# Optimization experiments

Hardware: AMD Instinct MI355X
Metric: run time of the kernel (lower is better)

The kernel has to match this reference:

```python
import jax, jax.numpy as jnp
import numpy as np
import math

B, S, D, H = 2, 2048, 1024, 16
DK = D // H


def setup_inputs() -> dict:
    key = jax.random.key(0)
    ks = jax.random.split(key, 12)
    std = 1.0 / math.sqrt(D)
    inp = {
        "q": jax.random.normal(ks[0], (B, S, D), jnp.float32),
        "k": jax.random.normal(ks[1], (B, S, D), jnp.float32),
        "v": jax.random.normal(ks[2], (B, S, D), jnp.float32),
        # causal mask, broadcast over batch and heads
        "mask": jnp.tril(jnp.ones((S, S), jnp.int32))[None, None, :, :],
        "wq": jax.random.normal(ks[3], (D, D), jnp.float32) * std,
        "bq": jax.random.normal(ks[4], (D,), jnp.float32) * std,
        "wk": jax.random.normal(ks[5], (D, D), jnp.float32) * std,
        "bk": jax.random.normal(ks[6], (D,), jnp.float32) * std,
        "wv": jax.random.normal(ks[7], (D, D), jnp.float32) * std,
        "bv": jax.random.normal(ks[8], (D,), jnp.float32) * std,
        "wo": jax.random.normal(ks[9], (D, D), jnp.float32) * std,
        "bo": jax.random.normal(ks[10], (D,), jnp.float32) * std,
    }
    return inp


def _split_heads(x):
    # [B,S,D] -> [B,H,S,DK]
    b, s, _ = x.shape
    return x.reshape(b, s, H, DK).transpose(0, 2, 1, 3)


def reference(q, k, v, mask, wq, bq, wk, bk, wv, bv, wo, bo):
    # nn.Linear: y = x @ W^T + b
    query = _split_heads(q @ wq.T + bq)
    key_h = _split_heads(k @ wk.T + bk)
    value = _split_heads(v @ wv.T + bv)

    scale = 1.0 / math.sqrt(DK)
    scores = jnp.einsum("bhqd,bhkd->bhqk", query, key_h) * scale  # [B,H,S,S]
    scores = jnp.where(mask == 0, jnp.float32(-1e9), scores)
    attn = jax.nn.softmax(scores, axis=-1)  # dropout p=0.0 -> identity

    x = jnp.einsum("bhqk,bhkd->bhqd", attn, value)  # [B,H,S,DK]
    x = x.transpose(0, 2, 1, 3).reshape(q.shape[0], -1, H * DK)  # [B,S,D]
    return x @ wo.T + bo
```

## Files before the change

kernel.cpp:

```cpp
#include <hip/hip_runtime.h>

#define B_SZ    2
#define S_LEN   2048
#define D_MODEL 1024
#define H_NUM   16
#define DK_H    64
#define M_ROWS  (B_SZ * S_LEN)

typedef __attribute__((ext_vector_type(8))) short  short8;
typedef __attribute__((ext_vector_type(4))) short  short4v;
typedef __attribute__((ext_vector_type(4))) float  floatx4;

__device__ __forceinline__ short f2b(float f) {
    union { float f; unsigned u; } x; x.f = f;
    unsigned u = x.u + 0x7fffu + ((x.u >> 16) & 1u);
    return (short)(u >> 16);
}

typedef __attribute__((address_space(1))) const unsigned int gu32;
typedef __attribute__((address_space(3))) unsigned int       lu32;
__device__ __forceinline__ void gload_lds16(const short* g, short* l) {
    __builtin_amdgcn_global_load_lds((gu32*)g, (lu32*)l, 16, 0, 0);
}

#define QSCALE 0.18033688011112042f
#define SM_SHIFT 12.0f

__global__ void cvt_all_kernel(const float* __restrict__ xq, const float* __restrict__ xk,
                               const float* __restrict__ xv, const float* __restrict__ wq,
                               const float* __restrict__ wk, const float* __restrict__ wv,
                               const float* __restrict__ wo,
                               short* __restrict__ oxq, short* __restrict__ oxk,
                               short* __restrict__ oxv, short* __restrict__ owq,
                               short* __restrict__ owk, short* __restrict__ owv,
                               short* __restrict__ owo)
{
    const int y = blockIdx.y;
    const float* in;
    short* out;
    switch (y) {
        case 0: in = xq; out = oxq; break;
        case 1: in = xk; out = oxk; break;
        case 2: in = xv; out = oxv; break;
        case 3: in = wq; out = owq; break;
        case 4: in = wk; out = owk; break;
        case 5: in = wv; out = owv; break;
        default: in = wo; out = owo; break;
    }
    if (y < 3) {
        int base = blockIdx.x * 1024 + threadIdx.x * 4;
        for (int p = 0; p < 4; ++p) {
            int i = base + p * 1048576;
            float4 v = *(const float4*)(in + i);
            short4v r;
            r[0] = f2b(v.x); r[1] = f2b(v.y); r[2] = f2b(v.z); r[3] = f2b(v.w);
            *(short4v*)(out + i) = r;
        }
    } else {
        int f = blockIdx.x * 256 + (int)threadIdx.x;
        if (blockIdx.x < 512) {
            int n4 = f >> 11, rem = f & 2047;
            int k8 = rem >> 4, nl = rem & 15;
            const float* src = in + (size_t)(n4 * 16 + nl) * D_MODEL + k8 * 8;
            float4 v0 = *(const float4*)(src);
            float4 v1 = *(const float4*)(src + 4);
            short8 r;
            r[0] = f2b(v0.x); r[1] = f2b(v0.y); r[2] = f2b(v0.z); r[3] = f2b(v0.w);
            r[4] = f2b(v1.x); r[5] = f2b(v1.y); r[6] = f2b(v1.z); r[7] = f2b(v1.w);
            *(short8*)(out + (size_t)f * 8) = r;
        }
    }
}

__global__ __launch_bounds__(256, 2)
void gemm_qkv_kernel(const short* __restrict__ xq, const short* __restrict__ xk,
                     const short* __restrict__ xv,
                     const short* __restrict__ wq, const short* __restrict__ wk,
                     const short* __restrict__ wv,
                     const float* __restrict__ bq, const float* __restrict__ bk,
                     const float* __restrict__ bv,
                     short* __restrict__ Qp, short* __restrict__ Kp, short* __restrict__ Vt)
{
    __shared__ short sa[2][128 * 64];

    const int which = blockIdx.y >> 3;
    const short* A    = (which == 0) ? xq : (which == 1) ? xk : xv;
    const short* W    = (which == 0) ? wq : (which == 1) ? wk : wv;
    const float* bias = (which == 0) ? bq : (which == 1) ? bk : bv;
    const float scale = (which == 0) ? QSCALE : 1.0f;

    const int nb = (blockIdx.y & 7) * 128;
    const int m0 = blockIdx.x * 128;
    const int t = threadIdx.x, wave = t >> 6, lane = t & 63;
    const int quad = lane >> 4, l16 = lane & 15;
    const int wm = (wave & 1) * 64, wn = (wave >> 1) * 64;

    const int rs = t >> 3;
    const int cl = (t & 7) ^ (rs & 7);
    const short* Asrc = A + (size_t)(m0 + rs) * D_MODEL + cl * 8;
    short* sd0 = &sa[0][t * 8];
    short* sd1 = &sa[1][t * 8];

#define STAGE_A(dst, k0) do { _Pragma("unroll")                                \
    for (int j_ = 0; j_ < 4; ++j_)                                             \
        gload_lds16(Asrc + (size_t)j_ * 32 * D_MODEL + (k0),                   \
                    (dst) + j_ * 2048); } while (0)

    int a_off[4][2];
#pragma unroll
    for (int i = 0; i < 4; ++i) {
        int ar = wm + i * 16 + l16;
#pragma unroll
        for (int ks = 0; ks < 2; ++ks)
            a_off[i][ks] = ar * 64 + (((ks * 4 + quad) ^ (ar & 7)) * 8);
    }

    const short* Wt = W + ((size_t)((nb + wn) >> 4) * 128 + quad) * 128 + l16 * 8;

#define LOADB(dst, k0) do { _Pragma("unroll")                                  \
    for (int nt_ = 0; nt_ < 4; ++nt_)                                          \
        dst[nt_] = *(const short8*)(Wt + nt_ * 16384 + (k0) * 16); } while (0)

    short8 bfA[4], bfB[4];
    STAGE_A(sd0, 0);
    LOADB(bfA, 0);
    __syncthreads();

    floatx4 acc[4][4] = {};
#pragma unroll 1
    for (int k0 = 0; k0 < D_MODEL; k0 += 64) {
        const int p = (k0 >> 6) & 1;
        const short* cur = &sa[p][0];
        if (k0 + 64 < D_MODEL) STAGE_A(p ? sd0 : sd1, k0 + 64);
        LOADB(bfB, k0 + 32);

        short8 af[4][2];
#pragma unroll
        for (int mt = 0; mt < 4; ++mt) {
            af[mt][0] = *(const short8*)(cur + a_off[mt][0]);
            af[mt][1] = *(const short8*)(cur + a_off[mt][1]);
        }
#pragma unroll
        for (int mt = 0; mt < 4; ++mt)
#pragma unroll
            for (int nt = 0; nt < 4; ++nt)
                acc[mt][nt] = __builtin_amdgcn_mfma_f32_16x16x32_bf16(af[mt][0], bfA[nt], acc[mt][nt], 0, 0, 0);
        if (k0 + 64 < D_MODEL) LOADB(bfA, k0 + 64);
#pragma unroll
        for (int mt = 0; mt < 4; ++mt)
#pragma unroll
            for (int nt = 0; nt < 4; ++nt)
                acc[mt][nt] = __builtin_amdgcn_mfma_f32_16x16x32_bf16(af[mt][1], bfB[nt], acc[mt][nt], 0, 0, 0);
        __syncthreads();
    }
#undef STAGE_A
#undef LOADB

#pragma unroll
    for (int nt = 0; nt < 4; ++nt) {
        int ncol = nb + wn + nt * 16 + l16;
        int h = ncol >> 6, dk = ncol & 63;
        float bv_ = bias[ncol];
#pragma unroll
        for (int mt = 0; mt < 4; ++mt) {
            int mrow0 = m0 + wm + mt * 16 + quad * 4;
            int bb = mrow0 >> 11, s0 = mrow0 & (S_LEN - 1);
            if (which < 2) {
                short* Out = (which == 0) ? Qp : Kp;
#pragma unroll
                for (int r = 0; r < 4; ++r) {
                    float v = (acc[mt][nt][r] + bv_) * scale;
                    Out[(((size_t)bb * H_NUM + h) * S_LEN + (s0 + r)) * DK_H + dk] = f2b(v);
                }
            } else {
                int Sb = s0 & ~63, sb0_ = s0 & 63;
                size_t rowbase = (((size_t)bb * H_NUM + h) * DK_H + dk) * S_LEN + Sb;
#pragma unroll
                for (int r = 0; r < 4; ++r) {
                    int cc = sb0_ + r;
                    Vt[rowbase + ((cc & 15) * 4 + (cc >> 4))] = f2b(acc[mt][nt][r] + bv_);
                }
            }
        }
    }
}

__global__ __launch_bounds__(512, 4)
void attn_kernel(const short* __restrict__ Qp, const short* __restrict__ Kp,
                 const short* __restrict__ Vt, short* __restrict__ Xa)
{
    __shared__ short kbuf[2][64 * 64];
    __shared__ short vbuf[2][64 * 64];
    __shared__ short pl[8][16 * 72];

    const int lin = (int)(blockIdx.x + 16 * blockIdx.y);
    const int bh = lin & 31;
    const int j8 = (lin >> 5) & 7;
    const int tile = (lin >> 8) ? (15 - j8) : j8;

    const int t = threadIdx.x, wave = t >> 6, lane = t & 63;
    const int quad = lane >> 4, l16 = lane & 15;

    const short* Qb  = Qp + (size_t)bh * S_LEN * DK_H;
    const short* Kb  = Kp + (size_t)bh * S_LEN * DK_H;
    const short* Vtb = Vt + (size_t)bh * DK_H * S_LEN;

    const int q0 = tile * 128 + wave * 16;
    const int my_ktimax = 2 * tile + (wave >> 2);
    const int ktb = 2 * tile + 1;

    const int r0 = t >> 3, cs = t & 7;
    const int c0 = cs ^ (r0 & 7);
    const short* Kg = Kb + r0 * DK_H + c0 * 8;
    const short* Vg = Vtb + (size_t)r0 * S_LEN + c0 * 8;
    short* kl0 = &kbuf[0][t * 8]; short* kl1 = &kbuf[1][t * 8];
    short* vl0 = &vbuf[0][t * 8]; short* vl1 = &vbuf[1][t * 8];

    short8 qf[2];
#pragma unroll
    for (int ks = 0; ks < 2; ++ks)
        qf[ks] = *(const short8*)(Qb + (size_t)(q0 + l16) * DK_H + ks * 32 + quad * 8);

    short8 bl = {};
    if (l16 == 0) {
#pragma unroll
        for (int j = 0; j < 8; ++j) bl[j] = (short)0x3F80;
    }

    int fo[4][2];
#pragma unroll
    for (int nt = 0; nt < 4; ++nt)
#pragma unroll
        for (int ks = 0; ks < 2; ++ks) {
            int row = nt * 16 + l16;
            fo[nt][ks] = row * 64 + (((ks * 4 + quad) ^ (l16 & 7)) * 8);
        }

    floatx4 o[4] = {};
    floatx4 ol = {};
    short* plw = &pl[wave][0];
    const int qg = q0 + quad * 4;

    gload_lds16(Kg, kl0);
    gload_lds16(Vg, vl0);
    __syncthreads();

    for (int kti = 0; kti <= ktb; ++kti) {
        const short* kb = (kti & 1) ? &kbuf[1][0] : &kbuf[0][0];
        const short* vb = (kti & 1) ? &vbuf[1][0] : &vbuf[0][0];
        const int kbase = kti * 64;

        if (kti < ktb) {
            gload_lds16(Kg + (size_t)(kbase + 64) * DK_H, (kti & 1) ? kl0 : kl1);
            gload_lds16(Vg + (kbase + 64),                (kti & 1) ? vl0 : vl1);
        }

        if (kti <= my_ktimax) {
            short8 bkf[4][2];
#pragma unroll
            for (int nt = 0; nt < 4; ++nt)
#pragma unroll
                for (int ks = 0; ks < 2; ++ks)
                    bkf[nt][ks] = *(const short8*)(kb + fo[nt][ks]);

            floatx4 sc[4] = {};
#pragma unroll
            for (int nt = 0; nt < 4; ++nt)
#pragma unroll
                for (int ks = 0; ks < 2; ++ks)
                    sc[nt] = __builtin_amdgcn_mfma_f32_16x16x32_bf16(qf[ks], bkf[nt][ks], sc[nt], 0, 0, 0);

            if (kti == my_ktimax) {
#pragma unroll
                for (int nt = 0; nt < 4; ++nt) {
                    int key = kbase + nt * 16 + l16;
#pragma unroll
                    for (int r = 0; r < 4; ++r)
                        if (key > qg + r) sc[nt][r] = -1e30f;
                }
            }

#pragma unroll
            for (int r = 0; r < 4; ++r) {
                union { float f; unsigned u; } a0, a1, a2, a3;
                a0.f = exp2f(sc[0][r] - SM_SHIFT);
                a1.f = exp2f(sc[1][r] - SM_SHIFT);
                a2.f = exp2f(sc[2][r] - SM_SHIFT);
                a3.f = exp2f(sc[3][r] - SM_SHIFT);
                uint2 d;
                d.x = (a1.u & 0xffff0000u) | (a0.u >> 16);
                d.y = (a3.u & 0xffff0000u) | (a2.u >> 16);
                *(uint2*)(plw + (quad * 4 + r) * 72 + l16 * 4) = d;
            }

            short8 ap0 = *(const short8*)(plw + l16 * 72 + quad * 8);
            short8 ap1 = *(const short8*)(plw + l16 * 72 + 32 + quad * 8);

            short8 bvf[4][2];
#pragma unroll
            for (int nt = 0; nt < 4; ++nt)
#pragma unroll
                for (int ks = 0; ks < 2; ++ks)
                    bvf[nt][ks] = *(const short8*)(vb + fo[nt][ks]);

#pragma unroll
            for (int nt = 0; nt < 4; ++nt) {
                o[nt] = __builtin_amdgcn_mfma_f32_16x16x32_bf16(ap0, bvf[nt][0], o[nt], 0, 0, 0);
                o[nt] = __builtin_amdgcn_mfma_f32_16x16x32_bf16(ap1, bvf[nt][1], o[nt], 0, 0, 0);
            }
            ol = __builtin_amdgcn_mfma_f32_16x16x32_bf16(ap0, bl, ol, 0, 0, 0);
            ol = __builtin_amdgcn_mfma_f32_16x16x32_bf16(ap1, bl, ol, 0, 0, 0);
        }

        __syncthreads();
    }

    const int b_ = bh >> 4, h = bh & 15;
#pragma unroll
    for (int r = 0; r < 4; ++r) {
        float lsum = __shfl(ol[r], (lane & 48));
        float rinv = 1.0f / lsum;
        int srow = qg + r;
#pragma unroll
        for (int nt = 0; nt < 4; ++nt) {
            int col = h * 64 + nt * 16 + l16;
            Xa[((size_t)b_ * S_LEN + srow) * D_MODEL + col] = f2b(o[nt][r] * rinv);
        }
    }
}

__global__ __launch_bounds__(256, 2)
void gemm_out_kernel(const short* __restrict__ A, const short* __restrict__ W,
                     const float* __restrict__ bias, float* __restrict__ out)
{
    __shared__ short sa[2][128 * 64];

    const int nb = blockIdx.y * 64;
    const int m0 = blockIdx.x * 128;
    const int t = threadIdx.x, wave = t >> 6, lane = t & 63;
    const int quad = lane >> 4, l16 = lane & 15;
    const int wm = (wave & 1) * 64, wn = (wave >> 1) * 32;

    const int rs = t >> 3;
    const int cl = (t & 7) ^ (rs & 7);
    const short* Asrc = A + (size_t)(m0 + rs) * D_MODEL + cl * 8;
    short* sd0 = &sa[0][t * 8];
    short* sd1 = &sa[1][t * 8];

#define STAGE_A(dst, k0) do { _Pragma("unroll")                                \
    for (int j_ = 0; j_ < 4; ++j_)                                             \
        gload_lds16(Asrc + (size_t)j_ * 32 * D_MODEL + (k0),                   \
                    (dst) + j_ * 2048); } while (0)

    int a_off[4][2];
#pragma unroll
    for (int i = 0; i < 4; ++i) {
        int ar = wm + i * 16 + l16;
#pragma unroll
        for (int ks = 0; ks < 2; ++ks)
            a_off[i][ks] = ar * 64 + (((ks * 4 + quad) ^ (ar & 7)) * 8);
    }

    const short* Wt = W + ((size_t)((nb + wn) >> 4) * 128 + quad) * 128 + l16 * 8;

#define LOADB2(dst, k0) do { _Pragma("unroll")                                 \
    for (int nt_ = 0; nt_ < 2; ++nt_)                                          \
        dst[nt_] = *(const short8*)(Wt + nt_ * 16384 + (k0) * 16); } while (0)

    short8 bfA[2], bfB[2];
    STAGE_A(sd0, 0);
    LOADB2(bfA, 0);
    __syncthreads();

    floatx4 acc[4][2] = {};
#pragma unroll 1
    for (int k0 = 0; k0 < D_MODEL; k0 += 64) {
        const int p = (k0 >> 6) & 1;
        const short* cur = &sa[p][0];
        if (k0 + 64 < D_MODEL) STAGE_A(p ? sd0 : sd1, k0 + 64);
        LOADB2(bfB, k0 + 32);

        short8 af[4][2];
#pragma unroll
        for (int mt = 0; mt < 4; ++mt) {
            af[mt][0] = *(const short8*)(cur + a_off[mt][0]);
            af[mt][1] = *(const short8*)(cur + a_off[mt][1]);
        }
#pragma unroll
        for (int mt = 0; mt < 4; ++mt)
#pragma unroll
            for (int nt = 0; nt < 2; ++nt)
                acc[mt][nt] = __builtin_amdgcn_mfma_f32_16x16x32_bf16(af[mt][0], bfA[nt], acc[mt][nt], 0, 0, 0);
        if (k0 + 64 < D_MODEL) LOADB2(bfA, k0 + 64);
#pragma unroll
        for (int mt = 0; mt < 4; ++mt)
#pragma unroll
            for (int nt = 0; nt < 2; ++nt)
                acc[mt][nt] = __builtin_amdgcn_mfma_f32_16x16x32_bf16(af[mt][1], bfB[nt], acc[mt][nt], 0, 0, 0);
        __syncthreads();
    }
#undef STAGE_A
#undef LOADB2

#pragma unroll
    for (int nt = 0; nt < 2; ++nt) {
        int ncol = nb + wn + nt * 16 + l16;
        float bv_ = bias[ncol];
#pragma unroll
        for (int mt = 0; mt < 4; ++mt) {
            int mrow0 = m0 + wm + mt * 16 + quad * 4;
#pragma unroll
            for (int r = 0; r < 4; ++r)
                out[(size_t)(mrow0 + r) * D_MODEL + ncol] = acc[mt][nt][r] + bv_;
        }
    }
}

extern "C" void kernel_launch(void* const* d_in, const int* in_sizes, int n_in,
                              void* d_out, int out_size, void* d_ws, size_t ws_size,
                              hipStream_t stream)
{
    (void)in_sizes; (void)n_in; (void)out_size; (void)ws_size;
    const float* q  = (const float*)d_in[0];
    const float* k  = (const float*)d_in[1];
    const float* v  = (const float*)d_in[2];
    const float* wq = (const float*)d_in[4];
    const float* bq = (const float*)d_in[5];
    const float* wk = (const float*)d_in[6];
    const float* bk = (const float*)d_in[7];
    const float* wv = (const float*)d_in[8];
    const float* bv = (const float*)d_in[9];
    const float* wo = (const float*)d_in[10];
    const float* bo = (const float*)d_in[11];
    float* out = (float*)d_out;

    const size_t XE = (size_t)M_ROWS * D_MODEL;
    const size_t WE = (size_t)D_MODEL * D_MODEL;
    short* ws_  = (short*)d_ws;
    short* xq_b = ws_;
    short* xk_b = xq_b + XE;
    short* xv_b = xk_b + XE;
    short* wq_b = xv_b + XE;
    short* wk_b = wq_b + WE;
    short* wv_b = wk_b + WE;
    short* wo_b = wv_b + WE;
    short* Qp   = wo_b + WE;
    short* Kp   = Qp + XE;
    short* Vt   = Kp + XE;
    short* Xa   = xq_b;

    dim3 blk(256);
    cvt_all_kernel<<<dim3(1024, 7), blk, 0, stream>>>(
        q, k, v, wq, wk, wv, wo, xq_b, xk_b, xv_b, wq_b, wk_b, wv_b, wo_b);

    gemm_qkv_kernel<<<dim3(M_ROWS / 128, 24), blk, 0, stream>>>(
        xq_b, xk_b, xv_b, wq_b, wk_b, wv_b, bq, bk, bv, Qp, Kp, Vt);

    attn_kernel<<<dim3(16, B_SZ * H_NUM), dim3(512), 0, stream>>>(Qp, Kp, Vt, Xa);

    gemm_out_kernel<<<dim3(M_ROWS / 128, D_MODEL / 64), blk, 0, stream>>>(Xa, wo_b, bo, out);
}
```

Measured before the change: 218.9 us.

## Fuse fp32-to-bf16 activation conversion into QKV GEMM A-tile loading

The separate pass that turned the q/k/v activations into bf16 in workspace is removed. The QKV GEMM now reads fp32 activations directly, converts them in registers and writes them into a single 32-wide LDS tile with a new swizzle. This saves a full read and write of three activation tensors. In exchange, the A loads become synchronous register round-trips with four barriers per 64-wide K step instead of async global-to-LDS double buffering, and occupancy is raised to three blocks per CU. The attention output buffer gets its own workspace region instead of aliasing the old bf16 q buffer.

```diff
diff --git a/kernel.cpp b/kernel.cpp
--- a/kernel.cpp
+++ b/kernel.cpp
@@ -26,65 +26,40 @@
 #define QSCALE 0.18033688011112042f
 #define SM_SHIFT 12.0f
 
-__global__ void cvt_all_kernel(const float* __restrict__ xq, const float* __restrict__ xk,
-                               const float* __restrict__ xv, const float* __restrict__ wq,
-                               const float* __restrict__ wk, const float* __restrict__ wv,
-                               const float* __restrict__ wo,
-                               short* __restrict__ oxq, short* __restrict__ oxk,
-                               short* __restrict__ oxv, short* __restrict__ owq,
-                               short* __restrict__ owk, short* __restrict__ owv,
-                               short* __restrict__ owo)
+__global__ void cvt_w_kernel(const float* __restrict__ wq, const float* __restrict__ wk,
+                             const float* __restrict__ wv, const float* __restrict__ wo,
+                             short* __restrict__ owq, short* __restrict__ owk,
+                             short* __restrict__ owv, short* __restrict__ owo)
 {
     const int y = blockIdx.y;
-    const float* in;
-    short* out;
-    switch (y) {
-        case 0: in = xq; out = oxq; break;
-        case 1: in = xk; out = oxk; break;
-        case 2: in = xv; out = oxv; break;
-        case 3: in = wq; out = owq; break;
-        case 4: in = wk; out = owk; break;
-        case 5: in = wv; out = owv; break;
-        default: in = wo; out = owo; break;
-    }
-    if (y < 3) {
-        int base = blockIdx.x * 1024 + threadIdx.x * 4;
-        for (int p = 0; p < 4; ++p) {
-            int i = base + p * 1048576;
-            float4 v = *(const float4*)(in + i);
-            short4v r;
-            r[0] = f2b(v.x); r[1] = f2b(v.y); r[2] = f2b(v.z); r[3] = f2b(v.w);
-            *(short4v*)(out + i) = r;
-        }
-    } else {
-        int f = blockIdx.x * 256 + (int)threadIdx.x;
-        if (blockIdx.x < 512) {
-            int n4 = f >> 11, rem = f & 2047;
-            int k8 = rem >> 4, nl = rem & 15;
-            const float* src = in + (size_t)(n4 * 16 + nl) * D_MODEL + k8 * 8;
-            float4 v0 = *(const float4*)(src);
-            float4 v1 = *(const float4*)(src + 4);
-            short8 r;
-            r[0] = f2b(v0.x); r[1] = f2b(v0.y); r[2] = f2b(v0.z); r[3] = f2b(v0.w);
-            r[4] = f2b(v1.x); r[5] = f2b(v1.y); r[6] = f2b(v1.z); r[7] = f2b(v1.w);
-            *(short8*)(out + (size_t)f * 8) = r;
-        }
-    }
-}
-
-__global__ __launch_bounds__(256, 2)
-void gemm_qkv_kernel(const short* __restrict__ xq, const short* __restrict__ xk,
-                     const short* __restrict__ xv,
+    const float* in = (y == 0) ? wq : (y == 1) ? wk : (y == 2) ? wv : wo;
+    short* out      = (y == 0) ? owq : (y == 1) ? owk : (y == 2) ? owv : owo;
+
+    int f = blockIdx.x * 256 + (int)threadIdx.x;
+    int n4 = f >> 11, rem = f & 2047;
+    int k8 = rem >> 4, nl = rem & 15;
+    const float* src = in + (size_t)(n4 * 16 + nl) * D_MODEL + k8 * 8;
+    float4 v0 = *(const float4*)(src);
+    float4 v1 = *(const float4*)(src + 4);
+    short8 r;
+    r[0] = f2b(v0.x); r[1] = f2b(v0.y); r[2] = f2b(v0.z); r[3] = f2b(v0.w);
+    r[4] = f2b(v1.x); r[5] = f2b(v1.y); r[6] = f2b(v1.z); r[7] = f2b(v1.w);
+    *(short8*)(out + (size_t)f * 8) = r;
+}
+
+__global__ __launch_bounds__(256, 3)
+void gemm_qkv_kernel(const float* __restrict__ xq, const float* __restrict__ xk,
+                     const float* __restrict__ xv,
                      const short* __restrict__ wq, const short* __restrict__ wk,
                      const short* __restrict__ wv,
                      const float* __restrict__ bq, const float* __restrict__ bk,
                      const float* __restrict__ bv,
                      short* __restrict__ Qp, short* __restrict__ Kp, short* __restrict__ Vt)
 {
-    __shared__ short sa[2][128 * 64];
+    __shared__ short sa[128 * 32];
 
     const int which = blockIdx.y >> 3;
-    const short* A    = (which == 0) ? xq : (which == 1) ? xk : xv;
+    const float* A    = (which == 0) ? xq : (which == 1) ? xk : xv;
     const short* W    = (which == 0) ? wq : (which == 1) ? wk : wv;
     const float* bias = (which == 0) ? bq : (which == 1) ? bk : bv;
     const float scale = (which == 0) ? QSCALE : 1.0f;
@@ -95,24 +70,32 @@
     const int quad = lane >> 4, l16 = lane & 15;
     const int wm = (wave & 1) * 64, wn = (wave >> 1) * 64;
 
-    const int rs = t >> 3;
-    const int cl = (t & 7) ^ (rs & 7);
-    const short* Asrc = A + (size_t)(m0 + rs) * D_MODEL + cl * 8;
-    short* sd0 = &sa[0][t * 8];
-    short* sd1 = &sa[1][t * 8];
-
-#define STAGE_A(dst, k0) do { _Pragma("unroll")                                \
-    for (int j_ = 0; j_ < 4; ++j_)                                             \
-        gload_lds16(Asrc + (size_t)j_ * 32 * D_MODEL + (k0),                   \
-                    (dst) + j_ * 2048); } while (0)
-
-    int a_off[4][2];
+    const int r0 = t >> 2, cs = t & 3;
+    const int c0 = cs ^ ((r0 >> 1) & 3);
+    const float* Af0 = A + (size_t)(m0 + r0) * D_MODEL + c0 * 8;
+    const float* Af1 = Af0 + (size_t)64 * D_MODEL;
+    short* sw0 = sa + t * 8;
+    short* sw1 = sa + 2048 + t * 8;
+
+    float4 g0a, g0b, g1a, g1b;
+#define ISSUE_A(k0) do {                                                       \
+    g0a = *(const float4*)(Af0 + (k0)); g0b = *(const float4*)(Af0 + (k0) + 4);\
+    g1a = *(const float4*)(Af1 + (k0)); g1b = *(const float4*)(Af1 + (k0) + 4);\
+} while (0)
+#define WRITE_A() do {                                                         \
+    short8 w0, w1;                                                             \
+    w0[0] = f2b(g0a.x); w0[1] = f2b(g0a.y); w0[2] = f2b(g0a.z); w0[3] = f2b(g0a.w); \
+    w0[4] = f2b(g0b.x); w0[5] = f2b(g0b.y); w0[6] = f2b(g0b.z); w0[7] = f2b(g0b.w); \
+    w1[0] = f2b(g1a.x); w1[1] = f2b(g1a.y); w1[2] = f2b(g1a.z); w1[3] = f2b(g1a.w); \
+    w1[4] = f2b(g1b.x); w1[5] = f2b(g1b.y); w1[6] = f2b(g1b.z); w1[7] = f2b(g1b.w); \
+    *(short8*)sw0 = w0; *(short8*)sw1 = w1;                                    \
+} while (0)
+
+    int a_off[4];
 #pragma unroll
     for (int i = 0; i < 4; ++i) {
         int ar = wm + i * 16 + l16;
-#pragma unroll
-        for (int ks = 0; ks < 2; ++ks)
-            a_off[i][ks] = ar * 64 + (((ks * 4 + quad) ^ (ar & 7)) * 8);
+        a_off[i] = ar * 32 + ((quad ^ ((ar >> 1) & 3)) * 8);
     }
 
     const short* Wt = W + ((size_t)((nb + wn) >> 4) * 128 + quad) * 128 + l16 * 8;
@@ -122,38 +105,39 @@
         dst[nt_] = *(const short8*)(Wt + nt_ * 16384 + (k0) * 16); } while (0)
 
     short8 bfA[4], bfB[4];
-    STAGE_A(sd0, 0);
+    ISSUE_A(0);
     LOADB(bfA, 0);
-    __syncthreads();
 
     floatx4 acc[4][4] = {};
 #pragma unroll 1
     for (int k0 = 0; k0 < D_MODEL; k0 += 64) {
-        const int p = (k0 >> 6) & 1;
-        const short* cur = &sa[p][0];
-        if (k0 + 64 < D_MODEL) STAGE_A(p ? sd0 : sd1, k0 + 64);
+        __syncthreads();
+        WRITE_A();
+        ISSUE_A(k0 + 32);
+        __syncthreads();
         LOADB(bfB, k0 + 32);
-
-        short8 af[4][2];
 #pragma unroll
         for (int mt = 0; mt < 4; ++mt) {
-            af[mt][0] = *(const short8*)(cur + a_off[mt][0]);
-            af[mt][1] = *(const short8*)(cur + a_off[mt][1]);
-        }
-#pragma unroll
-        for (int mt = 0; mt < 4; ++mt)
+            short8 af = *(const short8*)(sa + a_off[mt]);
 #pragma unroll
             for (int nt = 0; nt < 4; ++nt)
-                acc[mt][nt] = __builtin_amdgcn_mfma_f32_16x16x32_bf16(af[mt][0], bfA[nt], acc[mt][nt], 0, 0, 0);
+                acc[mt][nt] = __builtin_amdgcn_mfma_f32_16x16x32_bf16(af, bfA[nt], acc[mt][nt], 0, 0, 0);
+        }
+        __syncthreads();
+        WRITE_A();
+        if (k0 + 64 < D_MODEL) ISSUE_A(k0 + 64);
+        __syncthreads();
         if (k0 + 64 < D_MODEL) LOADB(bfA, k0 + 64);
 #pragma unroll
-        for (int mt = 0; mt < 4; ++mt)
+        for (int mt = 0; mt < 4; ++mt) {
+            short8 af = *(const short8*)(sa + a_off[mt]);
 #pragma unroll
             for (int nt = 0; nt < 4; ++nt)
-                acc[mt][nt] = __builtin_amdgcn_mfma_f32_16x16x32_bf16(af[mt][1], bfB[nt], acc[mt][nt], 0, 0, 0);
-        __syncthreads();
-    }
-#undef STAGE_A
+                acc[mt][nt] = __builtin_amdgcn_mfma_f32_16x16x32_bf16(af, bfB[nt], acc[mt][nt], 0, 0, 0);
+        }
+    }
+#undef ISSUE_A
+#undef WRITE_A
 #undef LOADB
 
 #pragma unroll
@@ -437,24 +421,21 @@
     const size_t XE = (size_t)M_ROWS * D_MODEL;
     const size_t WE = (size_t)D_MODEL * D_MODEL;
     short* ws_  = (short*)d_ws;
-    short* xq_b = ws_;
-    short* xk_b = xq_b + XE;
-    short* xv_b = xk_b + XE;
-    short* wq_b = xv_b + XE;
+    short* wq_b = ws_;
     short* wk_b = wq_b + WE;
     short* wv_b = wk_b + WE;
     short* wo_b = wv_b + WE;
     short* Qp   = wo_b + WE;
     short* Kp   = Qp + XE;
     short* Vt   = Kp + XE;
-    short* Xa   = xq_b;
+    short* Xa   = Vt + XE;
 
     dim3 blk(256);
-    cvt_all_kernel<<<dim3(1024, 7), blk, 0, stream>>>(
-        q, k, v, wq, wk, wv, wo, xq_b, xk_b, xv_b, wq_b, wk_b, wv_b, wo_b);
+    cvt_w_kernel<<<dim3(512, 4), blk, 0, stream>>>(
+        wq, wk, wv, wo, wq_b, wk_b, wv_b, wo_b);
 
     gemm_qkv_kernel<<<dim3(M_ROWS / 128, 24), blk, 0, stream>>>(
-        xq_b, xk_b, xv_b, wq_b, wk_b, wv_b, bq, bk, bv, Qp, Kp, Vt);
+        q, k, v, wq_b, wk_b, wv_b, bq, bk, bv, Qp, Kp, Vt);
 
     attn_kernel<<<dim3(16, B_SZ * H_NUM), dim3(512), 0, stream>>>(Qp, Kp, Vt, Xa);
 
```

Result: slower. 228.5 us (+4.4%).

## Replace double-buffered A staging with single 32-wide LDS buffer in QKV GEMM

Applied to the files above, without the earlier changes.

The QKV projection GEMM now stages A tiles into one 128x32 LDS buffer instead of two 128x64 ping-pong buffers, with a new XOR swizzle matched to the narrower tile. Each half-step of K is loaded and consumed in turn, separated by barriers. This cuts LDS use from 32KB to 8KB per block, which may allow more blocks per CU. In exchange it drops the overlap of global-to-LDS loads with MFMA compute and quadruples the number of barriers, so the loads are exposed.

```diff
diff --git a/kernel.cpp b/kernel.cpp
--- a/kernel.cpp
+++ b/kernel.cpp
@@ -81,7 +81,7 @@
                      const float* __restrict__ bv,
                      short* __restrict__ Qp, short* __restrict__ Kp, short* __restrict__ Vt)
 {
-    __shared__ short sa[2][128 * 64];
+    __shared__ short sa[128 * 32];
 
     const int which = blockIdx.y >> 3;
     const short* A    = (which == 0) ? xq : (which == 1) ? xk : xv;
@@ -95,24 +95,17 @@
     const int quad = lane >> 4, l16 = lane & 15;
     const int wm = (wave & 1) * 64, wn = (wave >> 1) * 64;
 
-    const int rs = t >> 3;
-    const int cl = (t & 7) ^ (rs & 7);
-    const short* Asrc = A + (size_t)(m0 + rs) * D_MODEL + cl * 8;
-    short* sd0 = &sa[0][t * 8];
-    short* sd1 = &sa[1][t * 8];
-
-#define STAGE_A(dst, k0) do { _Pragma("unroll")                                \
-    for (int j_ = 0; j_ < 4; ++j_)                                             \
-        gload_lds16(Asrc + (size_t)j_ * 32 * D_MODEL + (k0),                   \
-                    (dst) + j_ * 2048); } while (0)
-
-    int a_off[4][2];
+    const int r0 = t >> 2, cs = t & 3;
+    const int c0 = cs ^ ((r0 >> 1) & 3);
+    const short* Ab0 = A + (size_t)(m0 + r0) * D_MODEL + c0 * 8;
+    const short* Ab1 = Ab0 + (size_t)64 * D_MODEL;
+    short* sa0 = sa + t * 8;  short* sa1 = sa + 2048 + t * 8;
+
+    int a_off[4];
 #pragma unroll
     for (int i = 0; i < 4; ++i) {
         int ar = wm + i * 16 + l16;
-#pragma unroll
-        for (int ks = 0; ks < 2; ++ks)
-            a_off[i][ks] = ar * 64 + (((ks * 4 + quad) ^ (ar & 7)) * 8);
+        a_off[i] = ar * 32 + ((quad ^ ((ar >> 1) & 3)) * 8);
     }
 
     const short* Wt = W + ((size_t)((nb + wn) >> 4) * 128 + quad) * 128 + l16 * 8;
@@ -122,38 +115,36 @@
         dst[nt_] = *(const short8*)(Wt + nt_ * 16384 + (k0) * 16); } while (0)
 
     short8 bfA[4], bfB[4];
-    STAGE_A(sd0, 0);
     LOADB(bfA, 0);
-    __syncthreads();
 
     floatx4 acc[4][4] = {};
 #pragma unroll 1
     for (int k0 = 0; k0 < D_MODEL; k0 += 64) {
-        const int p = (k0 >> 6) & 1;
-        const short* cur = &sa[p][0];
-        if (k0 + 64 < D_MODEL) STAGE_A(p ? sd0 : sd1, k0 + 64);
+        __syncthreads();
+        gload_lds16(Ab0 + k0, sa0);
+        gload_lds16(Ab1 + k0, sa1);
+        __syncthreads();
         LOADB(bfB, k0 + 32);
-
-        short8 af[4][2];
 #pragma unroll
         for (int mt = 0; mt < 4; ++mt) {
-            af[mt][0] = *(const short8*)(cur + a_off[mt][0]);
-            af[mt][1] = *(const short8*)(cur + a_off[mt][1]);
-        }
-#pragma unroll
-        for (int mt = 0; mt < 4; ++mt)
+            short8 af = *(const short8*)(sa + a_off[mt]);
 #pragma unroll
             for (int nt = 0; nt < 4; ++nt)
-                acc[mt][nt] = __builtin_amdgcn_mfma_f32_16x16x32_bf16(af[mt][0], bfA[nt], acc[mt][nt], 0, 0, 0);
+                acc[mt][nt] = __builtin_amdgcn_mfma_f32_16x16x32_bf16(af, bfA[nt], acc[mt][nt], 0, 0, 0);
+        }
+        __syncthreads();
+        gload_lds16(Ab0 + k0 + 32, sa0);
+        gload_lds16(Ab1 + k0 + 32, sa1);
+        __syncthreads();
         if (k0 + 64 < D_MODEL) LOADB(bfA, k0 + 64);
 #pragma unroll
-        for (int mt = 0; mt < 4; ++mt)
+        for (int mt = 0; mt < 4; ++mt) {
+            short8 af = *(const short8*)(sa + a_off[mt]);
 #pragma unroll
             for (int nt = 0; nt < 4; ++nt)
-                acc[mt][nt] = __builtin_amdgcn_mfma_f32_16x16x32_bf16(af[mt][1], bfB[nt], acc[mt][nt], 0, 0, 0);
-        __syncthreads();
-    }
-#undef STAGE_A
+                acc[mt][nt] = __builtin_amdgcn_mfma_f32_16x16x32_bf16(af, bfB[nt], acc[mt][nt], 0, 0, 0);
+        }
+    }
 #undef LOADB
 
 #pragma unroll
```

Measured after the change: 221.1 us, median of 4. Within noise of the previous version (+1.0%).
